# Kernel tuning notes

Hardware: AMD Instinct MI355X
Metric: run time of the kernel (lower is better)

## Reference

```python
import jax, jax.numpy as jnp
import numpy as np

C = 128        # in_channels
N = 80000      # nodes per type (user, item)
E = 1000000    # edges per relation
L = 400000     # link labels


def _evolve_gcn(x_src, edge_index, n_dst, p, W0, Wih, Whh, bih, bhh):
    """EvolveGCNH layer: TopK pooling -> 1-step GRU weight evolution -> GCN."""
    # TopK pooling: score = x @ p / ||p||, keep top C nodes, gate by tanh(score)
    score = x_src @ p / (jnp.linalg.norm(p) + 1e-16)          # [N_src]
    top_vals, top_idx = jax.lax.top_k(score, x_src.shape[1])   # k = C
    X_tilde = x_src[top_idx] * jnp.tanh(top_vals)[:, None]     # [C, C]
    # One GRU step: 'batch' dim = C rows of X_tilde, hidden = current weight W0
    gi = X_tilde @ Wih.T + bih                                 # [C, 3C]
    gh = W0 @ Whh.T + bhh                                      # [C, 3C]
    i_r, i_z, i_n = jnp.split(gi, 3, axis=1)
    h_r, h_z, h_n = jnp.split(gh, 3, axis=1)
    r = jax.nn.sigmoid(i_r + h_r)
    z = jax.nn.sigmoid(i_z + h_z)
    n = jnp.tanh(i_n + r * h_n)
    W = (1.0 - z) * n + z * W0                                 # evolved weight [C, C]
    # GCN propagation with symmetric degree norm, no self loops
    xw = x_src @ W                                             # [N_src, C]
    row, col = edge_index[0], edge_index[1]
    ones = jnp.ones(row.shape[0], dtype=xw.dtype)
    deg_src = jax.ops.segment_sum(ones, row, num_segments=x_src.shape[0])
    deg_dst = jax.ops.segment_sum(ones, col, num_segments=n_dst)
    inv_s = jnp.where(deg_src > 0, jax.lax.rsqrt(jnp.maximum(deg_src, 1.0)), 0.0)
    inv_d = jnp.where(deg_dst > 0, jax.lax.rsqrt(jnp.maximum(deg_dst, 1.0)), 0.0)
    norm = inv_s[row] * inv_d[col]                             # [E]
    return jax.ops.segment_sum(xw[row] * norm[:, None], col, num_segments=n_dst)


def setup_inputs() -> dict:
    key = jax.random.key(0)
    ks = jax.random.split(key, 20)
    f = lambda i, shape, s: jax.random.normal(ks[i], shape, dtype=jnp.float32) * s
    s_w = 1.0 / np.sqrt(C)
    return {
        "x_user": f(0, (N, C), 1.0),
        "x_item": f(1, (N, C), 1.0),
        "edge_ui": jax.random.randint(ks[2], (2, E), 0, N),
        "edge_iu": jax.random.randint(ks[3], (2, E), 0, N),
        "edge_label_index": jax.random.randint(ks[4], (2, L), 0, N),
        "p_ui": f(5, (C,), s_w),
        "W0_ui": f(6, (C, C), s_w),
        "Wih_ui": f(7, (3 * C, C), s_w),
        "Whh_ui": f(8, (3 * C, C), s_w),
        "bih_ui": f(9, (3 * C,), s_w),
        "bhh_ui": f(10, (3 * C,), s_w),
        "p_iu": f(11, (C,), s_w),
        "W0_iu": f(12, (C, C), s_w),
        "Wih_iu": f(13, (3 * C, C), s_w),
        "Whh_iu": f(14, (3 * C, C), s_w),
        "bih_iu": f(15, (3 * C,), s_w),
        "bhh_iu": f(16, (3 * C,), s_w),
        "W_post": f(17, (C, 2), s_w),
        "b_post": f(18, (2,), s_w),
    }


def reference(x_user, x_item, edge_ui, edge_iu, edge_label_index,
              p_ui, W0_ui, Wih_ui, Whh_ui, bih_ui, bhh_ui,
              p_iu, W0_iu, Wih_iu, Whh_iu, bih_iu, bhh_iu,
              W_post, b_post):
    # HeteroConv: one EvolveGCNH per relation, outputs grouped by dst node type
    h_item = jax.nn.relu(_evolve_gcn(x_user, edge_ui, x_item.shape[0],
                                     p_ui, W0_ui, Wih_ui, Whh_ui, bih_ui, bhh_ui))
    h_user = jax.nn.relu(_evolve_gcn(x_item, edge_iu, x_user.shape[0],
                                     p_iu, W0_iu, Wih_iu, Whh_iu, bih_iu, bhh_iu))
    # Link scorer: gather endpoints, hadamard, linear(C->2), sum over last dim
    h_src = h_user[edge_label_index[0]]                        # [L, C]
    h_dst = h_item[edge_label_index[1]]                        # [L, C]
    h = (h_src * h_dst) @ W_post + b_post                      # [L, 2]
    return jnp.sum(h, axis=-1)                                 # [L]
```

## Files before the change

### kernel.cpp

```cpp
#include <hip/hip_runtime.h>
#include <hip/hip_fp16.h>

constexpr int KC    = 128;
constexpr int NBLK  = 2048;
constexpr int CAPA  = 1024;
constexpr int CBITS = 12;
constexpr int CSZ   = 1 << CBITS;

using half8   = __attribute__((ext_vector_type(8))) _Float16;
using float4v = __attribute__((ext_vector_type(4))) float;

__device__ __forceinline__ unsigned fkey(float s) {
  unsigned u = __float_as_uint(s);
  return (u & 0x80000000u) ? ~u : (u | 0x80000000u);
}

__global__ void k_scores(const float* __restrict__ xu, const float* __restrict__ xi,
                         const float* __restrict__ pu, const float* __restrict__ pi,
                         float* __restrict__ scores, unsigned* __restrict__ hist,
                         __half* __restrict__ x16, int N) {
  int gw = (int)((blockIdx.x * blockDim.x + threadIdx.x) >> 6);
  int lane = threadIdx.x & 63;
  if (gw >= 2 * N) return;
  int rel = gw >= N;
  int r = gw - rel * N;
  const float* x = rel ? xi : xu;
  const float* p = rel ? pi : pu;
  float2 xv = ((const float2*)(x + (size_t)r * KC))[lane];
  float2 pv = ((const float2*)p)[lane];
  *(__half2*)(x16 + (size_t)gw * KC + lane * 2) = __floats2half2_rn(xv.x, xv.y);
  float s = xv.x * pv.x + xv.y * pv.y;
#pragma unroll
  for (int off = 32; off; off >>= 1) s += __shfl_down(s, off, 64);
  if (lane == 0) {
    scores[gw] = s;
    atomicAdd(&hist[rel * 65536 + (fkey(s) >> 16)], 1u);
  }
}

__global__ __launch_bounds__(256) void k_cnt(const int* __restrict__ eui,
                                             const int* __restrict__ eiu,
                                             unsigned* __restrict__ cnts,
                                             int E, int N, int NBC, int chunk, int NTOT) {
  __shared__ unsigned hD[4 * 48], hS[4 * 48];
  int t = threadIdx.x, blk = blockIdx.x, w = t >> 6;
  for (int b = t; b < 4 * 48; b += 256) { hD[b] = 0; hS[b] = 0; }
  __syncthreads();
  int lo = blk * chunk, hi = min(2 * E, lo + chunk);
  for (int i = lo + t; i < hi; i += 256) {
    int rel = i >= E;
    const int* e = rel ? eiu : eui;
    int j = i - rel * E;
    atomicAdd(&hD[w * 48 + ((rel * N + e[E + j]) >> CBITS)], 1u);
    atomicAdd(&hS[w * 48 + ((rel * N + e[j]) >> CBITS)], 1u);
  }
  __syncthreads();
  for (int b = t; b < NBC; b += 256) {
    cnts[(size_t)blk * NBC + b] = hD[b] + hD[48 + b] + hD[96 + b] + hD[144 + b];
    cnts[(size_t)NTOT + (size_t)blk * NBC + b] =
        hS[b] + hS[48 + b] + hS[96 + b] + hS[144 + b];
  }
}

__global__ void k_scan1(const unsigned* __restrict__ cnts, unsigned* __restrict__ sc,
                        unsigned* __restrict__ bsum, int NTOT, int NBC, int SCB) {
  __shared__ unsigned sh[1024];
  int t = threadIdx.x;
  int seg = blockIdx.x / SCB, lb = blockIdx.x % SCB;
  int li = lb * 1024 + t;
  unsigned v = 0;
  if (li < NTOT) {
    int b = li >> 11, blk = li & (NBLK - 1);
    v = cnts[(size_t)seg * NTOT + (size_t)blk * NBC + b];
  }
  sh[t] = v; __syncthreads();
  for (int off = 1; off < 1024; off <<= 1) {
    unsigned add = (t >= off) ? sh[t - off] : 0;
    __syncthreads();
    sh[t] += add;
    __syncthreads();
  }
  if (li < NTOT) sc[(size_t)seg * NTOT + li] = sh[t] - v;
  if (t == 1023) bsum[blockIdx.x] = sh[1023];
}

__global__ void k_scan2(unsigned* __restrict__ bsum, int nb) {
  __shared__ unsigned sh[256];
  unsigned* bs = bsum + blockIdx.x * nb;
  int t = threadIdx.x;
  unsigned v = (t < nb) ? bs[t] : 0;
  sh[t] = v; __syncthreads();
  for (int off = 1; off < 256; off <<= 1) {
    unsigned add = (t >= off) ? sh[t - off] : 0;
    __syncthreads();
    sh[t] += add;
    __syncthreads();
  }
  if (t < nb) bs[t] = sh[t] - v;
}

__global__ __launch_bounds__(256) void k_part(const int* __restrict__ eui,
                                              const int* __restrict__ eiu,
                                              const unsigned* __restrict__ cnts,
                                              const unsigned* __restrict__ sc,
                                              const unsigned* __restrict__ bsum,
                                              unsigned* __restrict__ recsD,
                                              unsigned* __restrict__ recsS,
                                              int E, int N, int NBC, int chunk,
                                              int NTOT, int SCB) {
  __shared__ unsigned curD[64], curS[64], deltaD[64], deltaS[64];
  __shared__ unsigned stageD[CAPA], stageS[CAPA];
  __shared__ unsigned char bktD[CAPA], bktS[CAPA];
  int t = threadIdx.x, blk = blockIdx.x;
  if (t < 64) {
    unsigned v = (t < NBC) ? cnts[(size_t)blk * NBC + t] : 0;
    unsigned cum = v;
#pragma unroll
    for (int off = 1; off < 64; off <<= 1) {
      unsigned u = __shfl_up(cum, off, 64);
      if (t >= off) cum += u;
    }
    if (t < NBC) curD[t] = cum - v;
  } else if (t < 128) {
    int l = t - 64;
    unsigned v = (l < NBC) ? cnts[(size_t)NTOT + (size_t)blk * NBC + l] : 0;
    unsigned cum = v;
#pragma unroll
    for (int off = 1; off < 64; off <<= 1) {
      unsigned u = __shfl_up(cum, off, 64);
      if (l >= off) cum += u;
    }
    if (l < NBC) curS[l] = cum - v;
  }
  __syncthreads();
  if (t < NBC) {
    int li = t * NBLK + blk;
    deltaD[t] = sc[li] + bsum[li >> 10] - curD[t];
    deltaS[t] = sc[NTOT + li] + bsum[SCB + (li >> 10)] - curS[t];
  }
  __syncthreads();
  int lo = blk * chunk, hi = min(2 * E, lo + chunk);
  for (int i = lo + t; i < hi; i += 256) {
    int rel = i >= E;
    const int* e = rel ? eiu : eui;
    int j = i - rel * E;
    int src_g = rel * N + e[j];
    int dst_g = rel * N + e[E + j];
    int bD = dst_g >> CBITS;
    unsigned pD = atomicAdd(&curD[bD], 1u);
    stageD[pD] = (unsigned)src_g | ((unsigned)(dst_g & (CSZ - 1)) << 18);
    bktD[pD] = (unsigned char)bD;
    int bS = src_g >> CBITS;
    unsigned pS = atomicAdd(&curS[bS], 1u);
    stageS[pS] = (unsigned)(src_g & (CSZ - 1));
    bktS[pS] = (unsigned char)bS;
  }
  __syncthreads();
  int cnt = hi - lo;
  for (int j = t; j < cnt; j += 256) {
    recsD[deltaD[bktD[j]] + j] = stageD[j];
    recsS[deltaS[bktS[j]] + j] = stageS[j];
  }
}

__global__ __launch_bounds__(1024) void k_refine(const unsigned* __restrict__ sc,
                                                 const unsigned* __restrict__ bsum,
                                                 const unsigned* __restrict__ recsD,
                                                 const unsigned* __restrict__ recsS,
                                                 int* __restrict__ ssrc,
                                                 int* __restrict__ deg_dst,
                                                 int* __restrict__ endp,
                                                 int* __restrict__ deg_src,
                                                 int E, int NBC, int N2,
                                                 int NTOT, int SCB) {
  __shared__ unsigned hist[CSZ];
  __shared__ unsigned cur[CSZ];
  __shared__ unsigned tmp16[16];
  int t = threadIdx.x;
  int isS = blockIdx.x >= NBC;
  int c = blockIdx.x - (isS ? NBC : 0);
  size_t soff = isS ? (size_t)NTOT : 0;
  int bso = isS ? SCB : 0;
  int liLo = c * NBLK;
  int lo = (int)(sc[soff + liLo] + bsum[bso + (liLo >> 10)]);
  int hi;
  if (c + 1 < NBC) {
    int liHi = (c + 1) * NBLK;
    hi = (int)(sc[soff + liHi] + bsum[bso + (liHi >> 10)]);
  } else hi = 2 * E;
  for (int b = t; b < CSZ; b += 1024) hist[b] = 0;
  __syncthreads();
  if (isS) {
    for (int j = lo + t; j < hi; j += 1024)
      atomicAdd(&hist[recsS[j]], 1u);
    __syncthreads();
    for (int b = t; b < CSZ; b += 1024) {
      int node = c * CSZ + b;
      if (node < N2) deg_src[node] = (int)hist[b];
    }
  } else {
    for (int j = lo + t; j < hi; j += 1024)
      atomicAdd(&hist[recsD[j] >> 18], 1u);
    __syncthreads();
    unsigned loc[4], s = 0;
    int base = t * 4;
#pragma unroll
    for (int k = 0; k < 4; ++k) { unsigned v = hist[base + k]; loc[k] = s; s += v; }
    unsigned inc = s;
#pragma unroll
    for (int off = 1; off < 64; off <<= 1) {
      unsigned u = __shfl_up(inc, off, 64);
      if ((t & 63) >= off) inc += u;
    }
    int w = t >> 6;
    if ((t & 63) == 63) tmp16[w] = inc;
    __syncthreads();
    unsigned wbase = 0;
    for (int j = 0; j < 16; ++j) if (j < w) wbase += tmp16[j];
    unsigned exc = wbase + inc - s;
#pragma unroll
    for (int k = 0; k < 4; ++k) {
      unsigned e0 = exc + loc[k];
      cur[base + k] = e0;
      int node = c * CSZ + base + k;
      if (node < N2) {
        deg_dst[node] = (int)hist[base + k];
        endp[node] = lo + (int)(e0 + hist[base + k]);
      }
    }
    __syncthreads();
    for (int j = lo + t; j < hi; j += 1024) {
      unsigned rec = recsD[j];
      unsigned pos = atomicAdd(&cur[rec >> 18], 1u);
      ssrc[lo + (int)pos] = (int)(rec & 0x3FFFFu);
    }
  }
}

__global__ void k_thresh(const unsigned* __restrict__ hist, unsigned* __restrict__ ctrl) {
  const unsigned* h = hist + blockIdx.x * 65536;
  unsigned* c = ctrl + blockIdx.x * 8;
  __shared__ unsigned csum[1024];
  __shared__ int s_chunk;
  __shared__ unsigned s_above;
  int t = threadIdx.x;
  unsigned s = 0;
  int hi = 65536 - 64 * t;
  for (int b = hi - 64; b < hi; ++b) s += h[b];
  csum[t] = s;
  __syncthreads();
  for (int off = 1; off < 1024; off <<= 1) {
    unsigned add = (t >= off) ? csum[t - off] : 0;
    __syncthreads();
    csum[t] += add;
    __syncthreads();
  }
  unsigned above = (t == 0) ? 0u : csum[t - 1];
  if (csum[t] >= 128u && above < 128u) { s_chunk = t; s_above = above; }
  __syncthreads();
  int chi = 65536 - 64 * s_chunk;
  __shared__ unsigned bs[64];
  if (t < 64) bs[t] = h[chi - 1 - t];
  __syncthreads();
  if (t < 64) {
    unsigned v = bs[t], cum = v;
#pragma unroll
    for (int off = 1; off < 64; off <<= 1) {
      unsigned u = __shfl_up(cum, off, 64);
      if (t >= off) cum += u;
    }
    unsigned prev = cum - v;
    if (s_above + cum >= 128u && s_above + prev < 128u)
      c[0] = (unsigned)(chi - 1 - t);
  }
}

__global__ void k_compact(const float* __restrict__ scores, unsigned* __restrict__ ctrl,
                          int* __restrict__ cand_idx, float* __restrict__ cand_val, int N) {
  int i = blockIdx.x * blockDim.x + threadIdx.x;
  if (i >= 2 * N) return;
  int rel = i >= N;
  float s = scores[i];
  if ((fkey(s) >> 16) >= ctrl[rel * 8]) {
    unsigned pos = atomicAdd(&ctrl[rel * 8 + 1], 1u);
    if (pos < 2048u) {
      cand_idx[rel * 2048 + pos] = i - rel * N;
      cand_val[rel * 2048 + pos] = s;
    }
  }
}

__global__ void k_topk(const unsigned* __restrict__ ctrl,
                       const int* __restrict__ cand_idx, const float* __restrict__ cand_val,
                       const float* __restrict__ pu, const float* __restrict__ pi,
                       int* __restrict__ top_idx, float* __restrict__ top_tanh) {
  __shared__ float vals[2048];
  __shared__ int   idxs[2048];
  __shared__ float red[128];
  int rel = blockIdx.x, t = threadIdx.x;
  const float* p = rel ? pi : pu;
  int n = (int)ctrl[rel * 8 + 1]; if (n > 2048) n = 2048;
  for (int i = t; i < n; i += 128) {
    vals[i] = cand_val[rel * 2048 + i];
    idxs[i] = cand_idx[rel * 2048 + i];
  }
  float pv = p[t];
  red[t] = pv * pv;
  __syncthreads();
  for (int off = 64; off; off >>= 1) { if (t < off) red[t] += red[t + off]; __syncthreads(); }
  float pn = sqrtf(red[0]) + 1e-16f;
  for (int c = t; c < n; c += 128) {
    float v = vals[c]; int id = idxs[c];
    int rank = 0;
    for (int j = 0; j < n; ++j) {
      float vj = vals[j];
      rank += (vj > v) || (vj == v && idxs[j] < id);
    }
    if (rank < KC) {
      top_idx[rel * KC + rank] = id;
      top_tanh[rel * KC + rank] = tanhf(v / pn);
    }
  }
}

__global__ void k_gru(const float* __restrict__ xu, const float* __restrict__ xi,
                      const int* __restrict__ top_idx, const float* __restrict__ top_tanh,
                      const float* __restrict__ W0u, const float* __restrict__ W0i,
                      const float* __restrict__ Wihu, const float* __restrict__ Wihi,
                      const float* __restrict__ Whhu, const float* __restrict__ Whhi,
                      const float* __restrict__ bihu, const float* __restrict__ bihi,
                      const float* __restrict__ bhhu, const float* __restrict__ bhhi,
                      __half* __restrict__ Wt) {
  __shared__ float xt[KC], w0[KC];
  int rel = blockIdx.x >> 7, c = blockIdx.x & 127, k = threadIdx.x;
  const float* x   = rel ? xi   : xu;
  const float* W0  = rel ? W0i  : W0u;
  const float* Wih = rel ? Wihi : Wihu;
  const float* Whh = rel ? Whhi : Whhu;
  const float* bih = rel ? bihi : bihu;
  const float* bhh = rel ? bhhi : bhhu;
  xt[k] = x[(size_t)top_idx[rel * KC + c] * KC + k] * top_tanh[rel * KC + c];
  w0[k] = W0[c * KC + k];
  __syncthreads();
  float gir = bih[k], giz = bih[KC + k], gin = bih[2 * KC + k];
  float ghr = bhh[k], ghz = bhh[KC + k], ghn = bhh[2 * KC + k];
  const float* wr = Wih + (size_t)k * KC;
  const float* wz = Wih + (size_t)(KC + k) * KC;
  const float* wn = Wih + (size_t)(2 * KC + k) * KC;
  const float* vr = Whh + (size_t)k * KC;
  const float* vz = Whh + (size_t)(KC + k) * KC;
  const float* vn = Whh + (size_t)(2 * KC + k) * KC;
  for (int j = 0; j < KC; ++j) {
    float xj = xt[j], hj = w0[j];
    gir += xj * wr[j]; giz += xj * wz[j]; gin += xj * wn[j];
    ghr += hj * vr[j]; ghz += hj * vz[j]; ghn += hj * vn[j];
  }
  float r = 1.f / (1.f + expf(-(gir + ghr)));
  float z = 1.f / (1.f + expf(-(giz + ghz)));
  float nn = tanhf(gin + r * ghn);
  float w = (1.f - z) * nn + z * w0[k];
  Wt[(size_t)rel * KC * KC + (size_t)k * KC + c] = __float2half_rn(w);
}

__global__ __launch_bounds__(256) void k_gemm(const __half* __restrict__ x16,
                                              const __half* __restrict__ Wt,
                                              const int* __restrict__ deg_src,
                                              __half* __restrict__ xw, int N) {
  __shared__ __half Ws[KC * KC];
  __shared__ __half outs[64 * 136];
  int rel = (blockIdx.x * 64) >= N;
  int t = threadIdx.x;
  const uint4* wg = (const uint4*)(Wt + (size_t)rel * KC * KC);
#pragma unroll
  for (int i = 0; i < 8; ++i)
    ((uint4*)Ws)[t + 256 * i] = wg[t + 256 * i];
  __syncthreads();
// ... 34 lines not shown
    int rr = idx >> 4, cc = idx & 15;
    *(uint4*)(xw + gbase + (size_t)rr * KC + cc * 8) =
        *(const uint4*)(outs + (size_t)rr * 136 + cc * 8);
  }
}

__global__ void k_agg(const __half* __restrict__ xw, const int* __restrict__ ssrc,
                      const int* __restrict__ endp, const int* __restrict__ deg_dst,
                      __half* __restrict__ h, int n2) {
  int gw = (int)((blockIdx.x * blockDim.x + threadIdx.x) >> 6);
  if (gw >= n2) return;
  int lane = threadIdx.x & 63;
  int q = lane >> 4, l16 = lane & 15;
  int d = deg_dst[gw];
  int end = endp[gw], start = end - d;
  __half2 a0[4], a1[4];
  __half2 z = __floats2half2_rn(0.f, 0.f);
#pragma unroll
  for (int k = 0; k < 4; ++k) { a0[k] = z; a1[k] = z; }
  int i = start + q;
  for (; i + 4 < end; i += 8) {
    int r0 = ssrc[i], r1 = ssrc[i + 4];
    uint4 u0 = ((const uint4*)(xw + (size_t)r0 * KC))[l16];
    uint4 u1 = ((const uint4*)(xw + (size_t)r1 * KC))[l16];
    const __half2* p0 = (const __half2*)&u0;
    const __half2* p1 = (const __half2*)&u1;
#pragma unroll
    for (int k = 0; k < 4; ++k) {
      a0[k] = __hadd2(a0[k], p0[k]);
      a1[k] = __hadd2(a1[k], p1[k]);
    }
  }
  if (i < end) {
    int r = ssrc[i];
    uint4 u = ((const uint4*)(xw + (size_t)r * KC))[l16];
    const __half2* p = (const __half2*)&u;
#pragma unroll
    for (int k = 0; k < 4; ++k) a0[k] = __hadd2(a0[k], p[k]);
  }
  float f[8];
#pragma unroll
  for (int k = 0; k < 4; ++k) {
    float2 x0 = __half22float2(a0[k]);
    float2 x1 = __half22float2(a1[k]);
    f[2 * k] = x0.x + x1.x; f[2 * k + 1] = x0.y + x1.y;
  }
#pragma unroll
  for (int k = 0; k < 8; ++k) {
    f[k] += __shfl_xor(f[k], 16, 64);
    f[k] += __shfl_xor(f[k], 32, 64);
  }
  if (q == 0) {
    float invd = d > 0 ? rsqrtf((float)d) : 0.f;
    __half2 pk[4];
#pragma unroll
    for (int k = 0; k < 4; ++k)
      pk[k] = __floats2half2_rn(fmaxf(f[2 * k] * invd, 0.f),
                                fmaxf(f[2 * k + 1] * invd, 0.f));
    uint4 u;
    u.x = *(unsigned*)&pk[0]; u.y = *(unsigned*)&pk[1];
    u.z = *(unsigned*)&pk[2]; u.w = *(unsigned*)&pk[3];
    ((uint4*)(h + (size_t)gw * KC))[l16] = u;
  }
}

__global__ void k_links(const __half* __restrict__ h,
                        const int* __restrict__ srcs, const int* __restrict__ dsts,
                        const float* __restrict__ Wp, const float* __restrict__ bp,
                        float* __restrict__ out, int L, int N) {
  int gw = (int)((blockIdx.x * blockDim.x + threadIdx.x) >> 6);
  int lane = threadIdx.x & 63;
  int q = lane >> 4, l16 = lane & 15;
  int li = gw * 4 + q;
  if (li >= L) return;
  int s = srcs[li], dd = dsts[li];
  const __half* hu = h + (size_t)N * KC;
  uint4 ua = ((const uint4*)(hu + (size_t)s * KC))[l16];
  uint4 ub = ((const uint4*)(h + (size_t)dd * KC))[l16];
  const __half2* pa = (const __half2*)&ua;
  const __half2* pb = (const __half2*)&ub;
  float acc = 0.f;
#pragma unroll
  for (int k = 0; k < 4; ++k) {
    float2 fa = __half22float2(pa[k]);
    float2 fb = __half22float2(pb[k]);
    float4 w = ((const float4*)Wp)[l16 * 4 + k];
    acc += fa.x * fb.x * (w.x + w.y) + fa.y * fb.y * (w.z + w.w);
  }
#pragma unroll
  for (int off = 8; off; off >>= 1) acc += __shfl_xor(acc, off, 64);
  if (l16 == 0) out[li] = acc + bp[0] + bp[1];
}

extern "C" void kernel_launch(void* const* d_in, const int* in_sizes, int n_in,
                              void* d_out, int out_size, void* d_ws, size_t ws_size,
                              hipStream_t stream) {
  const float* x_user = (const float*)d_in[0];
  const float* x_item = (const float*)d_in[1];
  const int*   edge_ui = (const int*)d_in[2];
  const int*   edge_iu = (const int*)d_in[3];
  const int*   elab    = (const int*)d_in[4];
  const float* p_ui   = (const float*)d_in[5];
  const float* W0_ui  = (const float*)d_in[6];
  const float* Wih_ui = (const float*)d_in[7];
  const float* Whh_ui = (const float*)d_in[8];
  const float* bih_ui = (const float*)d_in[9];
// ... 35 lines not shown
  float*    cand_val = (float*)carve(2 * 2048 * 4);
  int*      top_idx  = (int*)carve(2 * KC * 4);
  float*    top_tanh = (float*)carve(2 * KC * 4);
  __half*   Wt16     = (__half*)carve(2 * KC * KC * 2);
  unsigned* cnts     = (unsigned*)carve((size_t)2 * NTOT * 4);
  unsigned* sc       = (unsigned*)carve((size_t)2 * NTOT * 4);
  unsigned* bsum     = (unsigned*)carve((size_t)2 * SCB * 4);
  unsigned* recsD    = (unsigned*)carve((size_t)2 * E * 4);
  unsigned* recsS    = (unsigned*)carve((size_t)2 * E * 4);
  int*      ssrc     = (int*)carve((size_t)2 * E * 4);
  int*      deg_dst  = (int*)carve((size_t)N2 * 4);
  int*      endp     = (int*)carve((size_t)N2 * 4);

  hipMemsetAsync(zbase, 0, zBytes, stream);

  k_scores<<<(N2 + 3) / 4, 256, 0, stream>>>(x_user, x_item, p_ui, p_iu, scores, hist,
                                             x16, N);
  k_cnt<<<NBLK, 256, 0, stream>>>(edge_ui, edge_iu, cnts, E, N, NBC, chunk, NTOT);
  k_scan1<<<2 * SCB, 1024, 0, stream>>>(cnts, sc, bsum, NTOT, NBC, SCB);
  k_scan2<<<2, 256, 0, stream>>>(bsum, SCB);
  k_part<<<NBLK, 256, 0, stream>>>(edge_ui, edge_iu, cnts, sc, bsum, recsD, recsS,
                                   E, N, NBC, chunk, NTOT, SCB);
  k_refine<<<2 * NBC, 1024, 0, stream>>>(sc, bsum, recsD, recsS, ssrc, deg_dst, endp,
                                         deg_src, E, NBC, N2, NTOT, SCB);

  k_thresh<<<2, 1024, 0, stream>>>(hist, ctrl);
  k_compact<<<(N2 + 255) / 256, 256, 0, stream>>>(scores, ctrl, cand_idx, cand_val, N);
  k_topk<<<2, 128, 0, stream>>>(ctrl, cand_idx, cand_val, p_ui, p_iu, top_idx, top_tanh);
  k_gru<<<2 * KC, KC, 0, stream>>>(x_user, x_item, top_idx, top_tanh,
                                   W0_ui, W0_iu, Wih_ui, Wih_iu, Whh_ui, Whh_iu,
                                   bih_ui, bih_iu, bhh_ui, bhh_iu, Wt16);

  k_gemm<<<N2 / 64, 256, 0, stream>>>(x16, Wt16, deg_src, xw, N);
  k_agg<<<(N2 + 3) / 4, 256, 0, stream>>>(xw, ssrc, endp, deg_dst, h, N2);
  k_links<<<((L + 3) / 4 + 3) / 4, 256, 0, stream>>>(h, elab, elab + L, W_post, b_post,
                                                     (float*)d_out, L, N);
}
```

Measured before the change: 460.7 us.

## Merge independent pipeline stages into shared launches and retune gather kernels

Pairs of independent kernels (edge counting with score computation, threshold with scan1, scan2 with compact, topk with partition, refine with GRU) are merged into single launches that branch on block index. This cuts the launch count from about eleven to eight and lets independent work run concurrently. The aggregation loop is widened to four accumulators with guarded loads, and the link scorer becomes a grid-stride loop with hoisted weights. The score pass also switches to 32-lane float4 reads. The trade-offs are higher register and shared-memory use in the merged kernels and lower occupancy for the 1024-thread refine/GRU launch.

```diff
diff --git a/kernel.cpp b/kernel.cpp
--- a/kernel.cpp
+++ b/kernel.cpp
@@ -15,351 +15,371 @@
   return (u & 0x80000000u) ? ~u : (u | 0x80000000u);
 }
 
-__global__ void k_scores(const float* __restrict__ xu, const float* __restrict__ xi,
-                         const float* __restrict__ pu, const float* __restrict__ pi,
-                         float* __restrict__ scores, unsigned* __restrict__ hist,
-                         __half* __restrict__ x16, int N) {
-  int gw = (int)((blockIdx.x * blockDim.x + threadIdx.x) >> 6);
-  int lane = threadIdx.x & 63;
-  if (gw >= 2 * N) return;
-  int rel = gw >= N;
-  int r = gw - rel * N;
-  const float* x = rel ? xi : xu;
-  const float* p = rel ? pi : pu;
-  float2 xv = ((const float2*)(x + (size_t)r * KC))[lane];
-  float2 pv = ((const float2*)p)[lane];
-  *(__half2*)(x16 + (size_t)gw * KC + lane * 2) = __floats2half2_rn(xv.x, xv.y);
-  float s = xv.x * pv.x + xv.y * pv.y;
-#pragma unroll
-  for (int off = 32; off; off >>= 1) s += __shfl_down(s, off, 64);
-  if (lane == 0) {
-    scores[gw] = s;
-    atomicAdd(&hist[rel * 65536 + (fkey(s) >> 16)], 1u);
-  }
-}
-
-__global__ __launch_bounds__(256) void k_cnt(const int* __restrict__ eui,
-                                             const int* __restrict__ eiu,
-                                             unsigned* __restrict__ cnts,
-                                             int E, int N, int NBC, int chunk, int NTOT) {
+__global__ __launch_bounds__(256) void m1_cnt_scores(
+    const int* __restrict__ eui, const int* __restrict__ eiu,
+    unsigned* __restrict__ cnts,
+    const float* __restrict__ xu, const float* __restrict__ xi,
+    const float* __restrict__ pu, const float* __restrict__ pi,
+    float* __restrict__ scores, unsigned* __restrict__ hist,
+    __half* __restrict__ x16,
+    int E, int N, int NBC, int chunk, int NTOT) {
   __shared__ unsigned hD[4 * 48], hS[4 * 48];
-  int t = threadIdx.x, blk = blockIdx.x, w = t >> 6;
-  for (int b = t; b < 4 * 48; b += 256) { hD[b] = 0; hS[b] = 0; }
-  __syncthreads();
-  int lo = blk * chunk, hi = min(2 * E, lo + chunk);
-  for (int i = lo + t; i < hi; i += 256) {
-    int rel = i >= E;
-    const int* e = rel ? eiu : eui;
-    int j = i - rel * E;
-    atomicAdd(&hD[w * 48 + ((rel * N + e[E + j]) >> CBITS)], 1u);
-    atomicAdd(&hS[w * 48 + ((rel * N + e[j]) >> CBITS)], 1u);
-  }
-  __syncthreads();
-  for (int b = t; b < NBC; b += 256) {
-    cnts[(size_t)blk * NBC + b] = hD[b] + hD[48 + b] + hD[96 + b] + hD[144 + b];
-    cnts[(size_t)NTOT + (size_t)blk * NBC + b] =
-        hS[b] + hS[48 + b] + hS[96 + b] + hS[144 + b];
-  }
-}
-
-__global__ void k_scan1(const unsigned* __restrict__ cnts, unsigned* __restrict__ sc,
-                        unsigned* __restrict__ bsum, int NTOT, int NBC, int SCB) {
-  __shared__ unsigned sh[1024];
   int t = threadIdx.x;
-  int seg = blockIdx.x / SCB, lb = blockIdx.x % SCB;
-  int li = lb * 1024 + t;
-  unsigned v = 0;
-  if (li < NTOT) {
-    int b = li >> 11, blk = li & (NBLK - 1);
-    v = cnts[(size_t)seg * NTOT + (size_t)blk * NBC + b];
-  }
-  sh[t] = v; __syncthreads();
-  for (int off = 1; off < 1024; off <<= 1) {
-    unsigned add = (t >= off) ? sh[t - off] : 0;
-    __syncthreads();
-    sh[t] += add;
-    __syncthreads();
-  }
-  if (li < NTOT) sc[(size_t)seg * NTOT + li] = sh[t] - v;
-  if (t == 1023) bsum[blockIdx.x] = sh[1023];
-}
-
-__global__ void k_scan2(unsigned* __restrict__ bsum, int nb) {
-  __shared__ unsigned sh[256];
-  unsigned* bs = bsum + blockIdx.x * nb;
+  if (blockIdx.x < NBLK) {
+    int blk = blockIdx.x, w = t >> 6;
+    for (int b = t; b < 4 * 48; b += 256) { hD[b] = 0; hS[b] = 0; }
+    __syncthreads();
+    int lo = blk * chunk, hi = min(2 * E, lo + chunk);
+    for (int i = lo + t; i < hi; i += 256) {
+      int rel = i >= E;
+      const int* e = rel ? eiu : eui;
+      int j = i - rel * E;
+      atomicAdd(&hD[w * 48 + ((rel * N + e[E + j]) >> CBITS)], 1u);
+      atomicAdd(&hS[w * 48 + ((rel * N + e[j]) >> CBITS)], 1u);
+    }
+    __syncthreads();
+    for (int b = t; b < NBC; b += 256) {
+      cnts[(size_t)blk * NBC + b] = hD[b] + hD[48 + b] + hD[96 + b] + hD[144 + b];
+      cnts[(size_t)NTOT + (size_t)blk * NBC + b] =
+          hS[b] + hS[48 + b] + hS[96 + b] + hS[144 + b];
+    }
+  } else {
+    int gw = (blockIdx.x - NBLK) * 8 + (t >> 5);
+    if (gw >= 2 * N) return;
+    int lane = t & 31;
+    int rel = gw >= N;
+    int r = gw - rel * N;
+    const float* x = rel ? xi : xu;
+    const float* p = rel ? pi : pu;
+    float4 xv = ((const float4*)(x + (size_t)r * KC))[lane];
+    float4 pv = ((const float4*)p)[lane];
+    __half2 h0 = __floats2half2_rn(xv.x, xv.y);
+    __half2 h1 = __floats2half2_rn(xv.z, xv.w);
+    uint2 u; u.x = *(unsigned*)&h0; u.y = *(unsigned*)&h1;
+    ((uint2*)(x16 + (size_t)gw * KC))[lane] = u;
+    float s = xv.x * pv.x + xv.y * pv.y + xv.z * pv.z + xv.w * pv.w;
+#pragma unroll
+    for (int off = 16; off; off >>= 1) s += __shfl_down(s, off, 32);
+    if (lane == 0) {
+      scores[gw] = s;
+      atomicAdd(&hist[rel * 65536 + (fkey(s) >> 16)], 1u);
+    }
+  }
+}
+
+__global__ __launch_bounds__(1024) void m2_thresh_scan1(
+    const unsigned* __restrict__ cnts, unsigned* __restrict__ sc,
+    unsigned* __restrict__ bsum, const unsigned* __restrict__ hist,
+    unsigned* __restrict__ ctrl, int NTOT, int NBC, int SCB) {
+  __shared__ __align__(16) unsigned smem[1024 + 64 + 2];
   int t = threadIdx.x;
-  unsigned v = (t < nb) ? bs[t] : 0;
-  sh[t] = v; __syncthreads();
-  for (int off = 1; off < 256; off <<= 1) {
-    unsigned add = (t >= off) ? sh[t - off] : 0;
-    __syncthreads();
-    sh[t] += add;
-    __syncthreads();
-  }
-  if (t < nb) bs[t] = sh[t] - v;
-}
-
-__global__ __launch_bounds__(256) void k_part(const int* __restrict__ eui,
-                                              const int* __restrict__ eiu,
-                                              const unsigned* __restrict__ cnts,
-                                              const unsigned* __restrict__ sc,
-                                              const unsigned* __restrict__ bsum,
-                                              unsigned* __restrict__ recsD,
-                                              unsigned* __restrict__ recsS,
-                                              int E, int N, int NBC, int chunk,
-                                              int NTOT, int SCB) {
-  __shared__ unsigned curD[64], curS[64], deltaD[64], deltaS[64];
-  __shared__ unsigned stageD[CAPA], stageS[CAPA];
-  __shared__ unsigned char bktD[CAPA], bktS[CAPA];
-  int t = threadIdx.x, blk = blockIdx.x;
-  if (t < 64) {
-    unsigned v = (t < NBC) ? cnts[(size_t)blk * NBC + t] : 0;
-    unsigned cum = v;
-#pragma unroll
-    for (int off = 1; off < 64; off <<= 1) {
-      unsigned u = __shfl_up(cum, off, 64);
-      if (t >= off) cum += u;
-    }
-    if (t < NBC) curD[t] = cum - v;
-  } else if (t < 128) {
-    int l = t - 64;
-    unsigned v = (l < NBC) ? cnts[(size_t)NTOT + (size_t)blk * NBC + l] : 0;
-    unsigned cum = v;
-#pragma unroll
-    for (int off = 1; off < 64; off <<= 1) {
-      unsigned u = __shfl_up(cum, off, 64);
-      if (l >= off) cum += u;
-    }
-    if (l < NBC) curS[l] = cum - v;
-  }
-  __syncthreads();
-  if (t < NBC) {
-    int li = t * NBLK + blk;
-    deltaD[t] = sc[li] + bsum[li >> 10] - curD[t];
-    deltaS[t] = sc[NTOT + li] + bsum[SCB + (li >> 10)] - curS[t];
-  }
-  __syncthreads();
-  int lo = blk * chunk, hi = min(2 * E, lo + chunk);
-  for (int i = lo + t; i < hi; i += 256) {
-    int rel = i >= E;
-    const int* e = rel ? eiu : eui;
-    int j = i - rel * E;
-    int src_g = rel * N + e[j];
-    int dst_g = rel * N + e[E + j];
-    int bD = dst_g >> CBITS;
-    unsigned pD = atomicAdd(&curD[bD], 1u);
-    stageD[pD] = (unsigned)src_g | ((unsigned)(dst_g & (CSZ - 1)) << 18);
-    bktD[pD] = (unsigned char)bD;
-    int bS = src_g >> CBITS;
-    unsigned pS = atomicAdd(&curS[bS], 1u);
-    stageS[pS] = (unsigned)(src_g & (CSZ - 1));
-    bktS[pS] = (unsigned char)bS;
-  }
-  __syncthreads();
-  int cnt = hi - lo;
-  for (int j = t; j < cnt; j += 256) {
-    recsD[deltaD[bktD[j]] + j] = stageD[j];
-    recsS[deltaS[bktS[j]] + j] = stageS[j];
-  }
-}
-
-__global__ __launch_bounds__(1024) void k_refine(const unsigned* __restrict__ sc,
-                                                 const unsigned* __restrict__ bsum,
-                                                 const unsigned* __restrict__ recsD,
-                                                 const unsigned* __restrict__ recsS,
-                                                 int* __restrict__ ssrc,
-                                                 int* __restrict__ deg_dst,
-                                                 int* __restrict__ endp,
-                                                 int* __restrict__ deg_src,
-                                                 int E, int NBC, int N2,
-                                                 int NTOT, int SCB) {
-  __shared__ unsigned hist[CSZ];
-  __shared__ unsigned cur[CSZ];
-  __shared__ unsigned tmp16[16];
+  if (blockIdx.x < 2) {
+    const unsigned* h = hist + blockIdx.x * 65536;
+    unsigned* c = ctrl + blockIdx.x * 8;
+    unsigned* csum = smem;
+    unsigned* bs = smem + 1024;
+    unsigned s = 0;
+    int hi = 65536 - 64 * t;
+    for (int b = hi - 64; b < hi; ++b) s += h[b];
+    csum[t] = s;
+    __syncthreads();
+    for (int off = 1; off < 1024; off <<= 1) {
+      unsigned add = (t >= off) ? csum[t - off] : 0;
+      __syncthreads();
+      csum[t] += add;
+      __syncthreads();
+    }
+    unsigned above = (t == 0) ? 0u : csum[t - 1];
+    if (csum[t] >= 128u && above < 128u) { smem[1088] = (unsigned)t; smem[1089] = above; }
+    __syncthreads();
+    int chi = 65536 - 64 * (int)smem[1088];
+    unsigned s_above = smem[1089];
+    if (t < 64) bs[t] = h[chi - 1 - t];
+    __syncthreads();
+    if (t < 64) {
+      unsigned v = bs[t], cum = v;
+#pragma unroll
+      for (int off = 1; off < 64; off <<= 1) {
+        unsigned u = __shfl_up(cum, off, 64);
+        if (t >= off) cum += u;
+      }
+      unsigned prev = cum - v;
+      if (s_above + cum >= 128u && s_above + prev < 128u)
+        c[0] = (unsigned)(chi - 1 - t);
+    }
+  } else {
+    int vb = blockIdx.x - 2;
+    unsigned* sh = smem;
+    int seg = vb / SCB, lb = vb % SCB;
+    int li = lb * 1024 + t;
+    unsigned v = 0;
+    if (li < NTOT) {
+      int b = li >> 11, blk = li & (NBLK - 1);
+      v = cnts[(size_t)seg * NTOT + (size_t)blk * NBC + b];
+    }
+    sh[t] = v; __syncthreads();
+    for (int off = 1; off < 1024; off <<= 1) {
+      unsigned add = (t >= off) ? sh[t - off] : 0;
+      __syncthreads();
+      sh[t] += add;
+      __syncthreads();
+    }
+    if (li < NTOT) sc[(size_t)seg * NTOT + li] = sh[t] - v;
+    if (t == 1023) bsum[vb] = sh[1023];
+  }
+}
+
+__global__ __launch_bounds__(256) void m3_scan2_compact(
+    unsigned* __restrict__ bsum, int nb,
+    const float* __restrict__ scores, unsigned* __restrict__ ctrl,
+    int* __restrict__ cand_idx, float* __restrict__ cand_val, int N) {
+  if (blockIdx.x < 2) {
+    __shared__ unsigned sh[256];
+    unsigned* bs = bsum + blockIdx.x * nb;
+    int t = threadIdx.x;
+    unsigned v = (t < nb) ? bs[t] : 0;
+    sh[t] = v; __syncthreads();
+    for (int off = 1; off < 256; off <<= 1) {
+      unsigned add = (t >= off) ? sh[t - off] : 0;
+      __syncthreads();
+      sh[t] += add;
+      __syncthreads();
+    }
+    if (t < nb) bs[t] = sh[t] - v;
+  } else {
+    int i = (blockIdx.x - 2) * 256 + threadIdx.x;
+    if (i >= 2 * N) return;
+    int rel = i >= N;
+    float s = scores[i];
+    if ((fkey(s) >> 16) >= ctrl[rel * 8]) {
+      unsigned pos = atomicAdd(&ctrl[rel * 8 + 1], 1u);
+      if (pos < 2048u) {
+        cand_idx[rel * 2048 + pos] = i - rel * N;
+        cand_val[rel * 2048 + pos] = s;
+      }
+    }
+  }
+}
+
+__global__ __launch_bounds__(256) void m4_topk_part(
+    const int* __restrict__ eui, const int* __restrict__ eiu,
+    const unsigned* __restrict__ cnts, const unsigned* __restrict__ sc,
+    const unsigned* __restrict__ bsum,
+    unsigned* __restrict__ recsD, unsigned* __restrict__ recsS,
+    const unsigned* __restrict__ ctrl,
+    const int* __restrict__ cand_idx, const float* __restrict__ cand_val,
+    const float* __restrict__ pu, const float* __restrict__ pi,
+    int* __restrict__ top_idx, float* __restrict__ top_tanh,
+    int E, int N, int NBC, int chunk, int NTOT, int SCB) {
+  __shared__ __align__(16) char smem[16896];
   int t = threadIdx.x;
-  int isS = blockIdx.x >= NBC;
-  int c = blockIdx.x - (isS ? NBC : 0);
-  size_t soff = isS ? (size_t)NTOT : 0;
-  int bso = isS ? SCB : 0;
-  int liLo = c * NBLK;
-  int lo = (int)(sc[soff + liLo] + bsum[bso + (liLo >> 10)]);
-  int hi;
-  if (c + 1 < NBC) {
-    int liHi = (c + 1) * NBLK;
-    hi = (int)(sc[soff + liHi] + bsum[bso + (liHi >> 10)]);
-  } else hi = 2 * E;
-  for (int b = t; b < CSZ; b += 1024) hist[b] = 0;
-  __syncthreads();
-  if (isS) {
-    for (int j = lo + t; j < hi; j += 1024)
-      atomicAdd(&hist[recsS[j]], 1u);
-    __syncthreads();
-    for (int b = t; b < CSZ; b += 1024) {
-      int node = c * CSZ + b;
-      if (node < N2) deg_src[node] = (int)hist[b];
+  if (blockIdx.x < 2) {
+    float* vals = (float*)smem;
+    int*   idxs = (int*)(smem + 8192);
+    float* red  = (float*)(smem + 16384);
+    int rel = blockIdx.x;
+    const float* p = rel ? pi : pu;
+    int n = (int)ctrl[rel * 8 + 1]; if (n > 2048) n = 2048;
+    for (int i = t; i < n; i += 256) {
+      vals[i] = cand_val[rel * 2048 + i];
+      idxs[i] = cand_idx[rel * 2048 + i];
+    }
+    if (t < 128) { float pv = p[t]; red[t] = pv * pv; }
+    __syncthreads();
+    for (int off = 64; off; off >>= 1) {
+      if (t < off) red[t] += red[t + off];
+      __syncthreads();
+    }
+    float pn = sqrtf(red[0]) + 1e-16f;
+    for (int c = t; c < n; c += 256) {
+      float v = vals[c]; int id = idxs[c];
+      int rank = 0;
+      for (int j = 0; j < n; ++j) {
+        float vj = vals[j];
+        rank += (vj > v) || (vj == v && idxs[j] < id);
+      }
+      if (rank < KC) {
+        top_idx[rel * KC + rank] = id;
+        top_tanh[rel * KC + rank] = tanhf(v / pn);
+      }
     }
   } else {
-    for (int j = lo + t; j < hi; j += 1024)
-      atomicAdd(&hist[recsD[j] >> 18], 1u);
-    __syncthreads();
-    unsigned loc[4], s = 0;
-    int base = t * 4;
-#pragma unroll
-    for (int k = 0; k < 4; ++k) { unsigned v = hist[base + k]; loc[k] = s; s += v; }
-    unsigned inc = s;
-#pragma unroll
-    for (int off = 1; off < 64; off <<= 1) {
-      unsigned u = __shfl_up(inc, off, 64);
-      if ((t & 63) >= off) inc += u;
-    }
-    int w = t >> 6;
-    if ((t & 63) == 63) tmp16[w] = inc;
-    __syncthreads();
-    unsigned wbase = 0;
-    for (int j = 0; j < 16; ++j) if (j < w) wbase += tmp16[j];
-    unsigned exc = wbase + inc - s;
-#pragma unroll
-    for (int k = 0; k < 4; ++k) {
-      unsigned e0 = exc + loc[k];
-      cur[base + k] = e0;
-      int node = c * CSZ + base + k;
-      if (node < N2) {
-        deg_dst[node] = (int)hist[base + k];
-        endp[node] = lo + (int)(e0 + hist[base + k]);
-      }
-    }
-    __syncthreads();
-    for (int j = lo + t; j < hi; j += 1024) {
-      unsigned rec = recsD[j];
-      unsigned pos = atomicAdd(&cur[rec >> 18], 1u);
-      ssrc[lo + (int)pos] = (int)(rec & 0x3FFFFu);
-    }
-  }
-}
-
-__global__ void k_thresh(const unsigned* __restrict__ hist, unsigned* __restrict__ ctrl) {
-  const unsigned* h = hist + blockIdx.x * 65536;
-  unsigned* c = ctrl + blockIdx.x * 8;
-  __shared__ unsigned csum[1024];
-  __shared__ int s_chunk;
-  __shared__ unsigned s_above;
+    unsigned* curD   = (unsigned*)smem;
+    unsigned* curS   = (unsigned*)(smem + 256);
+    unsigned* deltaD = (unsigned*)(smem + 512);
+    unsigned* deltaS = (unsigned*)(smem + 768);
+    unsigned* stageD = (unsigned*)(smem + 1024);
+    unsigned* stageS = (unsigned*)(smem + 5120);
+    unsigned char* bktD = (unsigned char*)(smem + 9216);
+    unsigned char* bktS = (unsigned char*)(smem + 10240);
+    int blk = blockIdx.x - 2;
+    if (t < 64) {
+      unsigned v = (t < NBC) ? cnts[(size_t)blk * NBC + t] : 0;
+      unsigned cum = v;
+#pragma unroll
+      for (int off = 1; off < 64; off <<= 1) {
+        unsigned u = __shfl_up(cum, off, 64);
+        if (t >= off) cum += u;
+      }
+      if (t < NBC) curD[t] = cum - v;
+    } else if (t < 128) {
+      int l = t - 64;
+      unsigned v = (l < NBC) ? cnts[(size_t)NTOT + (size_t)blk * NBC + l] : 0;
+      unsigned cum = v;
+#pragma unroll
+      for (int off = 1; off < 64; off <<= 1) {
+        unsigned u = __shfl_up(cum, off, 64);
+        if (l >= off) cum += u;
+      }
+      if (l < NBC) curS[l] = cum - v;
+    }
+    __syncthreads();
+    if (t < NBC) {
+      int li = t * NBLK + blk;
+      deltaD[t] = sc[li] + bsum[li >> 10] - curD[t];
+      deltaS[t] = sc[NTOT + li] + bsum[SCB + (li >> 10)] - curS[t];
+    }
+    __syncthreads();
+    int lo = blk * chunk, hi = min(2 * E, lo + chunk);
+    for (int i = lo + t; i < hi; i += 256) {
+      int rel = i >= E;
+      const int* e = rel ? eiu : eui;
+      int j = i - rel * E;
+      int src_g = rel * N + e[j];
+      int dst_g = rel * N + e[E + j];
+      int bD = dst_g >> CBITS;
+      unsigned pD = atomicAdd(&curD[bD], 1u);
+      stageD[pD] = (unsigned)src_g | ((unsigned)(dst_g & (CSZ - 1)) << 18);
+      bktD[pD] = (unsigned char)bD;
+      int bS = src_g >> CBITS;
+      unsigned pS = atomicAdd(&curS[bS], 1u);
+      stageS[pS] = (unsigned)(src_g & (CSZ - 1));
+      bktS[pS] = (unsigned char)bS;
+    }
+    __syncthreads();
+    int cnt = hi - lo;
+    for (int j = t; j < cnt; j += 256) {
+      recsD[deltaD[bktD[j]] + j] = stageD[j];
+      recsS[deltaS[bktS[j]] + j] = stageS[j];
+    }
+  }
+}
+
+__global__ __launch_bounds__(1024) void m5_refine_gru(
+    const unsigned* __restrict__ sc, const unsigned* __restrict__ bsum,
+    const unsigned* __restrict__ recsD, const unsigned* __restrict__ recsS,
+    int* __restrict__ ssrc, int* __restrict__ deg_dst, int* __restrict__ endp,
+    int* __restrict__ deg_src,
+    const float* __restrict__ xu, const float* __restrict__ xi,
+    const int* __restrict__ top_idx, const float* __restrict__ top_tanh,
+    const float* __restrict__ W0u, const float* __restrict__ W0i,
+    const float* __restrict__ Wihu, const float* __restrict__ Wihi,
+    const float* __restrict__ Whhu, const float* __restrict__ Whhi,
+    const float* __restrict__ bihu, const float* __restrict__ bihi,
+    const float* __restrict__ bhhu, const float* __restrict__ bhhi,
+    __half* __restrict__ Wt,
+    int E, int NBC, int N2, int NTOT, int SCB) {
+  __shared__ __align__(16) char smem[32832];
   int t = threadIdx.x;
-  unsigned s = 0;
-  int hi = 65536 - 64 * t;
-  for (int b = hi - 64; b < hi; ++b) s += h[b];
-  csum[t] = s;
-  __syncthreads();
-  for (int off = 1; off < 1024; off <<= 1) {
-    unsigned add = (t >= off) ? csum[t - off] : 0;
-    __syncthreads();
-    csum[t] += add;
-    __syncthreads();
-  }
-  unsigned above = (t == 0) ? 0u : csum[t - 1];
-  if (csum[t] >= 128u && above < 128u) { s_chunk = t; s_above = above; }
-  __syncthreads();
-  int chi = 65536 - 64 * s_chunk;
-  __shared__ unsigned bs[64];
-  if (t < 64) bs[t] = h[chi - 1 - t];
-  __syncthreads();
-  if (t < 64) {
-    unsigned v = bs[t], cum = v;
-#pragma unroll
-    for (int off = 1; off < 64; off <<= 1) {
-      unsigned u = __shfl_up(cum, off, 64);
-      if (t >= off) cum += u;
-    }
-    unsigned prev = cum - v;
-    if (s_above + cum >= 128u && s_above + prev < 128u)
-      c[0] = (unsigned)(chi - 1 - t);
-  }
-}
-
-__global__ void k_compact(const float* __restrict__ scores, unsigned* __restrict__ ctrl,
-                          int* __restrict__ cand_idx, float* __restrict__ cand_val, int N) {
-  int i = blockIdx.x * blockDim.x + threadIdx.x;
-  if (i >= 2 * N) return;
-  int rel = i >= N;
-  float s = scores[i];
-  if ((fkey(s) >> 16) >= ctrl[rel * 8]) {
-    unsigned pos = atomicAdd(&ctrl[rel * 8 + 1], 1u);
-    if (pos < 2048u) {
-      cand_idx[rel * 2048 + pos] = i - rel * N;
-      cand_val[rel * 2048 + pos] = s;
-    }
-  }
-}
-
-__global__ void k_topk(const unsigned* __restrict__ ctrl,
-                       const int* __restrict__ cand_idx, const float* __restrict__ cand_val,
-                       const float* __restrict__ pu, const float* __restrict__ pi,
-                       int* __restrict__ top_idx, float* __restrict__ top_tanh) {
-  __shared__ float vals[2048];
-  __shared__ int   idxs[2048];
-  __shared__ float red[128];
-  int rel = blockIdx.x, t = threadIdx.x;
-  const float* p = rel ? pi : pu;
-  int n = (int)ctrl[rel * 8 + 1]; if (n > 2048) n = 2048;
-  for (int i = t; i < n; i += 128) {
-    vals[i] = cand_val[rel * 2048 + i];
-    idxs[i] = cand_idx[rel * 2048 + i];
-  }
-  float pv = p[t];
-  red[t] = pv * pv;
-  __syncthreads();
-  for (int off = 64; off; off >>= 1) { if (t < off) red[t] += red[t + off]; __syncthreads(); }
-  float pn = sqrtf(red[0]) + 1e-16f;
-  for (int c = t; c < n; c += 128) {
-    float v = vals[c]; int id = idxs[c];
-    int rank = 0;
-    for (int j = 0; j < n; ++j) {
-      float vj = vals[j];
-      rank += (vj > v) || (vj == v && idxs[j] < id);
-    }
-    if (rank < KC) {
-      top_idx[rel * KC + rank] = id;
-      top_tanh[rel * KC + rank] = tanhf(v / pn);
-    }
-  }
-}
-
-__global__ void k_gru(const float* __restrict__ xu, const float* __restrict__ xi,
-                      const int* __restrict__ top_idx, const float* __restrict__ top_tanh,
-                      const float* __restrict__ W0u, const float* __restrict__ W0i,
-                      const float* __restrict__ Wihu, const float* __restrict__ Wihi,
-                      const float* __restrict__ Whhu, const float* __restrict__ Whhi,
-                      const float* __restrict__ bihu, const float* __restrict__ bihi,
-                      const float* __restrict__ bhhu, const float* __restrict__ bhhi,
-                      __half* __restrict__ Wt) {
-  __shared__ float xt[KC], w0[KC];
-  int rel = blockIdx.x >> 7, c = blockIdx.x & 127, k = threadIdx.x;
-  const float* x   = rel ? xi   : xu;
-  const float* W0  = rel ? W0i  : W0u;
-  const float* Wih = rel ? Wihi : Wihu;
-  const float* Whh = rel ? Whhi : Whhu;
-  const float* bih = rel ? bihi : bihu;
-  const float* bhh = rel ? bhhi : bhhu;
-  xt[k] = x[(size_t)top_idx[rel * KC + c] * KC + k] * top_tanh[rel * KC + c];
-  w0[k] = W0[c * KC + k];
-  __syncthreads();
-  float gir = bih[k], giz = bih[KC + k], gin = bih[2 * KC + k];
-  float ghr = bhh[k], ghz = bhh[KC + k], ghn = bhh[2 * KC + k];
-  const float* wr = Wih + (size_t)k * KC;
-  const float* wz = Wih + (size_t)(KC + k) * KC;
-  const float* wn = Wih + (size_t)(2 * KC + k) * KC;
-  const float* vr = Whh + (size_t)k * KC;
-  const float* vz = Whh + (size_t)(KC + k) * KC;
-  const float* vn = Whh + (size_t)(2 * KC + k) * KC;
-  for (int j = 0; j < KC; ++j) {
-    float xj = xt[j], hj = w0[j];
-    gir += xj * wr[j]; giz += xj * wz[j]; gin += xj * wn[j];
-    ghr += hj * vr[j]; ghz += hj * vz[j]; ghn += hj * vn[j];
-  }
-  float r = 1.f / (1.f + expf(-(gir + ghr)));
-  float z = 1.f / (1.f + expf(-(giz + ghz)));
-  float nn = tanhf(gin + r * ghn);
-  float w = (1.f - z) * nn + z * w0[k];
-  Wt[(size_t)rel * KC * KC + (size_t)k * KC + c] = __float2half_rn(w);
+  if ((int)blockIdx.x < 2 * NBC) {
+    unsigned* rh  = (unsigned*)smem;
+    unsigned* cur = (unsigned*)(smem + 16384);
+    unsigned* t16 = (unsigned*)(smem + 32768);
+    int isS = blockIdx.x >= NBC;
+    int c = blockIdx.x - (isS ? NBC : 0);
+    size_t soff = isS ? (size_t)NTOT : 0;
+    int bso = isS ? SCB : 0;
+    int liLo = c * NBLK;
+    int lo = (int)(sc[soff + liLo] + bsum[bso + (liLo >> 10)]);
+    int hi;
+    if (c + 1 < NBC) {
+      int liHi = (c + 1) * NBLK;
+      hi = (int)(sc[soff + liHi] + bsum[bso + (liHi >> 10)]);
+    } else hi = 2 * E;
+    for (int b = t; b < CSZ; b += 1024) rh[b] = 0;
+    __syncthreads();
+    if (isS) {
+      for (int j = lo + t; j < hi; j += 1024)
+        atomicAdd(&rh[recsS[j]], 1u);
+      __syncthreads();
+      for (int b = t; b < CSZ; b += 1024) {
+        int node = c * CSZ + b;
+        if (node < N2) deg_src[node] = (int)rh[b];
+      }
+    } else {
+      for (int j = lo + t; j < hi; j += 1024)
+        atomicAdd(&rh[recsD[j] >> 18], 1u);
+      __syncthreads();
+      unsigned loc[4], s = 0;
+      int base = t * 4;
+#pragma unroll
+      for (int k = 0; k < 4; ++k) { unsigned v = rh[base + k]; loc[k] = s; s += v; }
+      unsigned inc = s;
+#pragma unroll
+      for (int off = 1; off < 64; off <<= 1) {
+        unsigned u = __shfl_up(inc, off, 64);
+        if ((t & 63) >= off) inc += u;
+      }
+      int w = t >> 6;
+      if ((t & 63) == 63) t16[w] = inc;
+      __syncthreads();
+      unsigned wbase = 0;
+      for (int j = 0; j < 16; ++j) if (j < w) wbase += t16[j];
+      unsigned exc = wbase + inc - s;
+#pragma unroll
+      for (int k = 0; k < 4; ++k) {
+        unsigned e0 = exc + loc[k];
+        cur[base + k] = e0;
+        int node = c * CSZ + base + k;
+        if (node < N2) {
+          deg_dst[node] = (int)rh[base + k];
+          endp[node] = lo + (int)(e0 + rh[base + k]);
+        }
+      }
+      __syncthreads();
+      for (int j = lo + t; j < hi; j += 1024) {
+        unsigned rec = recsD[j];
+        unsigned pos = atomicAdd(&cur[rec >> 18], 1u);
+        ssrc[lo + (int)pos] = (int)(rec & 0x3FFFFu);
+      }
+    }
+  } else {
+    int gb = blockIdx.x - 2 * NBC;
+    int rel = gb >> 7, c = gb & 127;
+    const float* x   = rel ? xi   : xu;
+    const float* W0  = rel ? W0i  : W0u;
+    const float* Wih = rel ? Wihi : Wihu;
+    const float* Whh = rel ? Whhi : Whhu;
+    const float* bih = rel ? bihi : bihu;
+    const float* bhh = rel ? bhhi : bhhu;
+    float* xt = (float*)smem;
+    float* w0 = (float*)(smem + 512);
+    if (t < KC) {
+      xt[t] = x[(size_t)top_idx[rel * KC + c] * KC + t] * top_tanh[rel * KC + c];
+      w0[t] = W0[c * KC + t];
+    }
+    __syncthreads();
+    if (t >= KC) return;
+    int k = t;
+    float gir = bih[k], giz = bih[KC + k], gin = bih[2 * KC + k];
+    float ghr = bhh[k], ghz = bhh[KC + k], ghn = bhh[2 * KC + k];
+    const float* wr = Wih + (size_t)k * KC;
+    const float* wz = Wih + (size_t)(KC + k) * KC;
+    const float* wn = Wih + (size_t)(2 * KC + k) * KC;
+    const float* vr = Whh + (size_t)k * KC;
+    const float* vz = Whh + (size_t)(KC + k) * KC;
+    const float* vn = Whh + (size_t)(2 * KC + k) * KC;
+    for (int j = 0; j < KC; ++j) {
+      float xj = xt[j], hj = w0[j];
+      gir += xj * wr[j]; giz += xj * wz[j]; gin += xj * wn[j];
+      ghr += hj * vr[j]; ghz += hj * vz[j]; ghn += hj * vn[j];
+    }
+    float r = 1.f / (1.f + expf(-(gir + ghr)));
+    float z = 1.f / (1.f + expf(-(giz + ghz)));
+    float nn = tanhf(gin + r * ghn);
+    float w = (1.f - z) * nn + z * w0[k];
+    Wt[(size_t)rel * KC * KC + (size_t)k * KC + c] = __float2half_rn(w);
+  }
 }
 
 __global__ __launch_bounds__(256) void k_gemm(const __half* __restrict__ x16,
@@ -424,36 +444,52 @@
   int q = lane >> 4, l16 = lane & 15;
   int d = deg_dst[gw];
   int end = endp[gw], start = end - d;
-  __half2 a0[4], a1[4];
   __half2 z = __floats2half2_rn(0.f, 0.f);
-#pragma unroll
-  for (int k = 0; k < 4; ++k) { a0[k] = z; a1[k] = z; }
-  int i = start + q;
-  for (; i + 4 < end; i += 8) {
-    int r0 = ssrc[i], r1 = ssrc[i + 4];
+  __half2 a0[4], a1[4], a2[4], a3[4];
+#pragma unroll
+  for (int k = 0; k < 4; ++k) { a0[k] = z; a1[k] = z; a2[k] = z; a3[k] = z; }
+  for (int i = start + q; i < end; i += 16) {
+    int i1 = i + 4, i2 = i + 8, i3 = i + 12;
+    bool b1 = i1 < end, b2 = i2 < end, b3 = i3 < end;
+    int r0 = ssrc[i], r1, r2, r3;
+    if (b1) r1 = ssrc[i1];
+    if (b2) r2 = ssrc[i2];
+    if (b3) r3 = ssrc[i3];
     uint4 u0 = ((const uint4*)(xw + (size_t)r0 * KC))[l16];
-    uint4 u1 = ((const uint4*)(xw + (size_t)r1 * KC))[l16];
-    const __half2* p0 = (const __half2*)&u0;
-    const __half2* p1 = (const __half2*)&u1;
-#pragma unroll
-    for (int k = 0; k < 4; ++k) {
-      a0[k] = __hadd2(a0[k], p0[k]);
-      a1[k] = __hadd2(a1[k], p1[k]);
-    }
-  }
-  if (i < end) {
-    int r = ssrc[i];
-    uint4 u = ((const uint4*)(xw + (size_t)r * KC))[l16];
-    const __half2* p = (const __half2*)&u;
-#pragma unroll
-    for (int k = 0; k < 4; ++k) a0[k] = __hadd2(a0[k], p[k]);
+    uint4 u1, u2, u3;
+    if (b1) u1 = ((const uint4*)(xw + (size_t)r1 * KC))[l16];
+    if (b2) u2 = ((const uint4*)(xw + (size_t)r2 * KC))[l16];
+    if (b3) u3 = ((const uint4*)(xw + (size_t)r3 * KC))[l16];
+    {
+      const __half2* p = (const __half2*)&u0;
+#pragma unroll
+      for (int k = 0; k < 4; ++k) a0[k] = __hadd2(a0[k], p[k]);
+    }
+    if (b1) {
+      const __half2* p = (const __half2*)&u1;
+#pragma unroll
+      for (int k = 0; k < 4; ++k) a1[k] = __hadd2(a1[k], p[k]);
+    }
+    if (b2) {
+      const __half2* p = (const __half2*)&u2;
+#pragma unroll
+      for (int k = 0; k < 4; ++k) a2[k] = __hadd2(a2[k], p[k]);
+    }
+    if (b3) {
+      const __half2* p = (const __half2*)&u3;
+#pragma unroll
+      for (int k = 0; k < 4; ++k) a3[k] = __hadd2(a3[k], p[k]);
+    }
   }
   float f[8];
 #pragma unroll
   for (int k = 0; k < 4; ++k) {
     float2 x0 = __half22float2(a0[k]);
     float2 x1 = __half22float2(a1[k]);
-    f[2 * k] = x0.x + x1.x; f[2 * k + 1] = x0.y + x1.y;
+    float2 x2 = __half22float2(a2[k]);
+    float2 x3 = __half22float2(a3[k]);
+    f[2 * k]     = (x0.x + x1.x) + (x2.x + x3.x);
+    f[2 * k + 1] = (x0.y + x1.y) + (x2.y + x3.y);
   }
 #pragma unroll
   for (int k = 0; k < 8; ++k) {
@@ -478,28 +514,36 @@
                         const int* __restrict__ srcs, const int* __restrict__ dsts,
                         const float* __restrict__ Wp, const float* __restrict__ bp,
                         float* __restrict__ out, int L, int N) {
-  int gw = (int)((blockIdx.x * blockDim.x + threadIdx.x) >> 6);
+  int tid = blockIdx.x * blockDim.x + threadIdx.x;
   int lane = threadIdx.x & 63;
   int q = lane >> 4, l16 = lane & 15;
-  int li = gw * 4 + q;
-  if (li >= L) return;
-  int s = srcs[li], dd = dsts[li];
+  int gq = (tid >> 6) * 4 + q;
+  int nq = (int)((gridDim.x * blockDim.x) >> 6) * 4;
+  float w8[8];
+#pragma unroll
+  for (int k = 0; k < 4; ++k) {
+    float4 w = ((const float4*)Wp)[l16 * 4 + k];
+    w8[2 * k] = w.x + w.y; w8[2 * k + 1] = w.z + w.w;
+  }
+  float bs = bp[0] + bp[1];
   const __half* hu = h + (size_t)N * KC;
-  uint4 ua = ((const uint4*)(hu + (size_t)s * KC))[l16];
-  uint4 ub = ((const uint4*)(h + (size_t)dd * KC))[l16];
-  const __half2* pa = (const __half2*)&ua;
-  const __half2* pb = (const __half2*)&ub;
-  float acc = 0.f;
-#pragma unroll
-  for (int k = 0; k < 4; ++k) {
-    float2 fa = __half22float2(pa[k]);
-    float2 fb = __half22float2(pb[k]);
-    float4 w = ((const float4*)Wp)[l16 * 4 + k];
-    acc += fa.x * fb.x * (w.x + w.y) + fa.y * fb.y * (w.z + w.w);
-  }
-#pragma unroll
-  for (int off = 8; off; off >>= 1) acc += __shfl_xor(acc, off, 64);
-  if (l16 == 0) out[li] = acc + bp[0] + bp[1];
+  for (int li = gq; li < L; li += nq) {
+    int s = srcs[li], dd = dsts[li];
+    uint4 ua = ((const uint4*)(hu + (size_t)s * KC))[l16];
+    uint4 ub = ((const uint4*)(h + (size_t)dd * KC))[l16];
+    const __half2* pa = (const __half2*)&ua;
+    const __half2* pb = (const __half2*)&ub;
+    float acc = 0.f;
+#pragma unroll
+    for (int k = 0; k < 4; ++k) {
+      float2 fa = __half22float2(pa[k]);
+      float2 fb = __half22float2(pb[k]);
+      acc += fa.x * fb.x * w8[2 * k] + fa.y * fb.y * w8[2 * k + 1];
+    }
+#pragma unroll
+    for (int off = 8; off; off >>= 1) acc += __shfl_xor(acc, off, 64);
+    if (l16 == 0) out[li] = acc + bs;
+  }
 }
 
 extern "C" void kernel_launch(void* const* d_in, const int* in_sizes, int n_in,
@@ -565,25 +609,28 @@
 
   hipMemsetAsync(zbase, 0, zBytes, stream);
 
-  k_scores<<<(N2 + 3) / 4, 256, 0, stream>>>(x_user, x_item, p_ui, p_iu, scores, hist,
-                                             x16, N);
-  k_cnt<<<NBLK, 256, 0, stream>>>(edge_ui, edge_iu, cnts, E, N, NBC, chunk, NTOT);
-  k_scan1<<<2 * SCB, 1024, 0, stream>>>(cnts, sc, bsum, NTOT, NBC, SCB);
-  k_scan2<<<2, 256, 0, stream>>>(bsum, SCB);
-  k_part<<<NBLK, 256, 0, stream>>>(edge_ui, edge_iu, cnts, sc, bsum, recsD, recsS,
-                                   E, N, NBC, chunk, NTOT, SCB);
-  k_refine<<<2 * NBC, 1024, 0, stream>>>(sc, bsum, recsD, recsS, ssrc, deg_dst, endp,
-                                         deg_src, E, NBC, N2, NTOT, SCB);
-
-  k_thresh<<<2, 1024, 0, stream>>>(hist, ctrl);
-  k_compact<<<(N2 + 255) / 256, 256, 0, stream>>>(scores, ctrl, cand_idx, cand_val, N);
-  k_topk<<<2, 128, 0, stream>>>(ctrl, cand_idx, cand_val, p_ui, p_iu, top_idx, top_tanh);
-  k_gru<<<2 * KC, KC, 0, stream>>>(x_user, x_item, top_idx, top_tanh,
-                                   W0_ui, W0_iu, Wih_ui, Wih_iu, Whh_ui, Whh_iu,
-                                   bih_ui, bih_iu, bhh_ui, bhh_iu, Wt16);
-
+  const int SBLK = (N2 + 7) / 8;
+  m1_cnt_scores<<<NBLK + SBLK, 256, 0, stream>>>(edge_ui, edge_iu, cnts,
+                                                 x_user, x_item, p_ui, p_iu,
+                                                 scores, hist, x16,
+                                                 E, N, NBC, chunk, NTOT);
+  m2_thresh_scan1<<<2 + 2 * SCB, 1024, 0, stream>>>(cnts, sc, bsum, hist, ctrl,
+                                                    NTOT, NBC, SCB);
+  m3_scan2_compact<<<2 + (N2 + 255) / 256, 256, 0, stream>>>(bsum, SCB, scores, ctrl,
+                                                             cand_idx, cand_val, N);
+  m4_topk_part<<<2 + NBLK, 256, 0, stream>>>(edge_ui, edge_iu, cnts, sc, bsum,
+                                             recsD, recsS, ctrl, cand_idx, cand_val,
+                                             p_ui, p_iu, top_idx, top_tanh,
+                                             E, N, NBC, chunk, NTOT, SCB);
+  m5_refine_gru<<<2 * NBC + 2 * KC, 1024, 0, stream>>>(sc, bsum, recsD, recsS, ssrc,
+                                                       deg_dst, endp, deg_src,
+                                                       x_user, x_item, top_idx, top_tanh,
+                                                       W0_ui, W0_iu, Wih_ui, Wih_iu,
+                                                       Whh_ui, Whh_iu, bih_ui, bih_iu,
+                                                       bhh_ui, bhh_iu, Wt16,
+                                                       E, NBC, N2, NTOT, SCB);
   k_gemm<<<N2 / 64, 256, 0, stream>>>(x16, Wt16, deg_src, xw, N);
   k_agg<<<(N2 + 3) / 4, 256, 0, stream>>>(xw, ssrc, endp, deg_dst, h, N2);
-  k_links<<<((L + 3) / 4 + 3) / 4, 256, 0, stream>>>(h, elab, elab + L, W_post, b_post,
-                                                     (float*)d_out, L, N);
-}
+  k_links<<<2048, 256, 0, stream>>>(h, elab, elab + L, W_post, b_post,
+                                    (float*)d_out, L, N);
+}
```

Result: faster. 424.9 us (-7.8%).
